# Optimization experiments

Measured on AMD Instinct MI355X. Metric: run time of the kernel, lower is better.

The kernel has to match this reference:

```python
import jax, jax.numpy as jnp
import numpy as np

NEG = -1e9

def _lstm_dir(x, w_ih, w_hh, b_ih, b_hh):
    # x: (N, T, in) -> (N, T, H); torch gate order i, f, g, o
    xi = x @ w_ih.T + (b_ih + b_hh)  # (N, T, 4H) input projection precomputed
    H = w_hh.shape[1]
    h0 = jnp.zeros((x.shape[0], H), x.dtype)
    def step(carry, xt):
        h, c = carry
        g = xt + h @ w_hh.T
        i, f, gg, o = jnp.split(g, 4, axis=-1)
        c = jax.nn.sigmoid(f) * c + jax.nn.sigmoid(i) * jnp.tanh(gg)
        h = jax.nn.sigmoid(o) * jnp.tanh(c)
        return (h, c), h
    _, ys = jax.lax.scan(step, (h0, h0), jnp.swapaxes(xi, 0, 1))
    return jnp.swapaxes(ys, 0, 1)

def _bilstm_layer(x, wif, whf, bif, bhf, wib, whb, bib, bhb):
    fwd = _lstm_dir(x, wif, whf, bif, bhf)
    bwd = _lstm_dir(x[:, ::-1], wib, whb, bib, bhb)[:, ::-1]
    return jnp.concatenate([fwd, bwd], axis=-1)

def _na1d(x, qkv_w, qkv_b, rpb, proj_w, proj_b, heads, kernel):
    # NATTEN-style 1D neighborhood attention with edge-clamped window + rel pos bias.
    N, L, Dm = x.shape
    hd = Dm // heads
    qkv = x @ qkv_w.T + qkv_b
    q, k, v = jnp.split(qkv, 3, axis=-1)
    sh = lambda t: t.reshape(N, L, heads, hd).transpose(0, 2, 1, 3)
    q, k, v = sh(q) * (hd ** -0.5), sh(k), sh(v)
    scores = jnp.einsum('nhid,nhjd->nhij', q, k)  # (N, heads, L, L)
    i = jnp.arange(L)[:, None]
    j = jnp.arange(L)[None, :]
    start = jnp.clip(i - kernel // 2, 0, L - kernel)     # window start per query
    mask = (j >= start) & (j < start + kernel)           # (L, L) neighborhood mask
    rel = jnp.clip(j - i + kernel - 1, 0, 2 * kernel - 2)
    bias = rpb[:, rel]                                   # (heads, L, L)
    scores = jnp.where(mask, scores + bias, NEG)
    attn = jax.nn.softmax(scores, axis=-1)
    out = jnp.einsum('nhij,nhjd->nhid', attn, v)
    out = out.transpose(0, 2, 1, 3).reshape(N, L, Dm)
    return out @ proj_w.T + proj_b

def setup_inputs() -> dict:
    key = jax.random.key(0)
    ks = iter(jax.random.split(key, 40))
    B, IN, T, P, Dm, H = 4, 256, 256, 88, 128, 64
    p = lambda *s: jax.random.normal(next(ks), s, jnp.float32) * 0.05
    inp = {'x': jax.random.normal(next(ks), (B, IN, T, P), jnp.float32)}
    for l, fin in (('l0', IN), ('l1', Dm)):
        for suf in ('', 'r'):
            inp['w_ih_' + l + suf] = p(4 * H, fin)
            inp['w_hh_' + l + suf] = p(4 * H, H)
            inp['b_ih_' + l + suf] = p(4 * H)
            inp['b_hh_' + l + suf] = p(4 * H)
    for tag, kz in (('t', 7), ('f', 87)):
        inp['qkv_w_' + tag] = p(3 * Dm, Dm)
        inp['qkv_b_' + tag] = p(3 * Dm)
        inp['rpb_' + tag] = p(1, 2 * kz - 1)
        inp['proj_w_' + tag] = p(Dm, Dm)
        inp['proj_b_' + tag] = p(Dm)
    return inp

def reference(x, w_ih_l0, w_hh_l0, b_ih_l0, b_hh_l0, w_ih_l0r, w_hh_l0r, b_ih_l0r, b_hh_l0r, w_ih_l1, w_hh_l1, b_ih_l1, b_hh_l1, w_ih_l1r, w_hh_l1r, b_ih_l1r, b_hh_l1r, qkv_w_t, qkv_b_t, rpb_t, proj_w_t, proj_b_t, qkv_w_f, qkv_b_f, rpb_f, proj_w_f, proj_b_f):
    B, IN, T, P = x.shape
    Dm = proj_w_t.shape[0]
    h = jnp.transpose(x, (0, 3, 2, 1)).reshape(B * P, T, IN)
    h = _bilstm_layer(h, w_ih_l0, w_hh_l0, b_ih_l0, b_hh_l0, w_ih_l0r, w_hh_l0r, b_ih_l0r, b_hh_l0r)
    h = _bilstm_layer(h, w_ih_l1, w_hh_l1, b_ih_l1, b_hh_l1, w_ih_l1r, w_hh_l1r, b_ih_l1r, b_hh_l1r)
    h = _na1d(h, qkv_w_t, qkv_b_t, rpb_t, proj_w_t, proj_b_t, 1, 7)            # time axis
    h = h.reshape(B, P, T, Dm).transpose(0, 2, 1, 3).reshape(B * T, P, Dm)
    h = _na1d(h, qkv_w_f, qkv_b_f, rpb_f, proj_w_f, proj_b_f, 1, 87)           # pitch axis
    return h.reshape(B, T, P, Dm)
```

## Files before the change

kernel.cpp:

```cpp
#include <hip/hip_runtime.h>
#include <cstdint>

#define TP 22528
#define MROWS 90112

typedef __bf16 bf16x8 __attribute__((ext_vector_type(8)));
typedef float  f32x4  __attribute__((ext_vector_type(4)));
typedef unsigned short ushort8 __attribute__((ext_vector_type(8)));

__device__ __forceinline__ unsigned short f2bf(float x) {
    unsigned u = __builtin_bit_cast(unsigned, x);
    return (unsigned short)((u + 0x7fffu + ((u >> 16) & 1u)) >> 16);
}
__device__ __forceinline__ float bf2f(unsigned short h) {
    return __builtin_bit_cast(float, (unsigned)h << 16);
}
__device__ __forceinline__ void gl16(const void* g, void* l) {
    __builtin_amdgcn_global_load_lds(
        (const __attribute__((address_space(1))) void*)g,
        (__attribute__((address_space(3))) void*)l, 16, 0, 0);
}

__global__ void convert_w(const float* __restrict__ s0, const float* __restrict__ s1,
                          const float* __restrict__ s2, const float* __restrict__ s3,
                          const float* __restrict__ s4, const float* __restrict__ s5,
                          const float* __restrict__ s6, const float* __restrict__ s7,
                          unsigned short* __restrict__ WH, unsigned short* __restrict__ WL)
{
    const int stride = gridDim.x * blockDim.x;
    for (int i = blockIdx.x * blockDim.x + threadIdx.x; i < 327680; i += stride) {
        const float* s; int base;
        if      (i <  65536) { s = s0; base = 0; }
        else if (i < 131072) { s = s1; base = 65536; }
        else if (i < 163840) { s = s2; base = 131072; }
        else if (i < 196608) { s = s3; base = 163840; }
        else if (i < 245760) { s = s4; base = 196608; }
        else if (i < 262144) { s = s5; base = 245760; }
        else if (i < 311296) { s = s6; base = 262144; }
        else                 { s = s7; base = 311296; }
        const float v = s[i - base];
        const unsigned short h = f2bf(v);
        WH[i] = h; WL[i] = f2bf(v - bf2f(h));
    }
}

__launch_bounds__(256)
__global__ void transpose_x(const float* __restrict__ x,
                            unsigned short* __restrict__ Xh,
                            unsigned short* __restrict__ Xl)
{
    __shared__ float tile[64][65];
    const int tid = threadIdx.x;
    const int tp0 = blockIdx.x * 64, k0 = blockIdx.y * 64, b = blockIdx.z;
    #pragma unroll
    for (int i = 0; i < 16; ++i) {
        const int idx = i * 256 + tid;
        const int kl = idx >> 6, tpl = idx & 63;
        tile[kl][tpl] = x[(size_t)(b * 256 + k0 + kl) * TP + tp0 + tpl];
    }
    __syncthreads();
    #pragma unroll
    for (int i = 0; i < 2; ++i) {
        const int u = i * 2048 + tid * 8;
        const int ml = u >> 6, kl0 = u & 63;
        ushort8 hi, lo;
        #pragma unroll
        for (int j = 0; j < 8; ++j) {
            const float v = tile[kl0 + j][ml];
            const unsigned short h = f2bf(v);
            hi[j] = h; lo[j] = f2bf(v - bf2f(h));
        }
        const size_t row = (size_t)b * TP + tp0 + ml;
        *(ushort8*)&Xh[row * 256 + k0 + kl0] = hi;
        *(ushort8*)&Xl[row * 256 + k0 + kl0] = lo;
    }
}

template<int OUTBF>
__launch_bounds__(256, 2)
__global__ void gemm_bf16(const unsigned short* __restrict__ Ahi,
                          const unsigned short* __restrict__ Alo,
                          const unsigned short* __restrict__ Whi0,
                          const unsigned short* __restrict__ Wlo0,
                          const unsigned short* __restrict__ Whi1,
                          const unsigned short* __restrict__ Wlo1,
                          const float* __restrict__ b0a, const float* __restrict__ b0b,
                          const float* __restrict__ b1a, const float* __restrict__ b1b,
                          float* __restrict__ C,
                          unsigned short* __restrict__ Chi, unsigned short* __restrict__ Clo,
                          int ldc, int K, int splitN, int NB)
{
    __shared__ unsigned short lds[32768];
    const int tid  = threadIdx.x;
    const int bid  = blockIdx.x;
    const int q8   = (int)gridDim.x >> 3;
    const int wq   = (bid & 7) * q8 + (bid >> 3);
    const int nb   = wq % NB;
    const int mb   = wq / NB;
    const int n0   = nb * 128;
    const int m0   = mb * 128;
    const unsigned short* Wh; const unsigned short* Wl;
    const float* ba; const float* bb; int nr0;
    if (n0 < splitN) { Wh = Whi0; Wl = Wlo0; ba = b0a; bb = b0b; nr0 = n0; }
    else             { Wh = Whi1; Wl = Wlo1; ba = b1a; bb = b1b; nr0 = n0 - splitN; }
    const int lane = tid & 63;
    const int wv   = tid >> 6;
    const int wm   = wv >> 1, wn = wv & 1;
    const int lr   = lane & 15, lg = lane >> 4;
    const int voff = (lane >> 2) * K + (((lane & 3) ^ ((lane >> 2) & 3)) * 8);
    const int wb   = wv * 1024;

    const unsigned short* gAh = Ahi + (size_t)(m0 + wv * 32) * K + voff;
    const unsigned short* gAl = Alo + (size_t)(m0 + wv * 32) * K + voff;
    const unsigned short* gBh = Wh + (size_t)(nr0 + wv * 32) * K + voff;
    const unsigned short* gBl = Wl + (size_t)(nr0 + wv * 32) * K + voff;

    const int NT = K >> 5;
    f32x4 acc[4][4] = {};

    auto stage = [&](int bufi, int ks) {
        unsigned short* base = lds + bufi * 16384;
        gl16(gAh + ks,          base +         wb);
        gl16(gAh + ks + 16 * K, base +         wb + 512);
        gl16(gAl + ks,          base + 4096  + wb);
        gl16(gAl + ks + 16 * K, base + 4096  + wb + 512);
        gl16(gBh + ks,          base + 8192  + wb);
        gl16(gBh + ks + 16 * K, base + 8192  + wb + 512);
        gl16(gBl + ks,          base + 12288 + wb);
        gl16(gBl + ks + 16 * K, base + 12288 + wb + 512);
    };

    stage(0, 0);
    for (int t = 0; t < NT; ++t) {
        const int cur = (t & 1) * 16384;
        if (t + 1 < NT) {
            stage((t & 1) ^ 1, (t + 1) * 32);
            asm volatile("s_waitcnt vmcnt(8)" ::: "memory");
        } else {
            asm volatile("s_waitcnt vmcnt(0)" ::: "memory");
        }
        __builtin_amdgcn_s_barrier();
        __builtin_amdgcn_sched_barrier(0);
        bf16x8 ah[4], al[4], bh[4], bl[4];
        #pragma unroll
        for (int mf = 0; mf < 4; ++mf) {
            const int r = wm * 64 + mf * 16 + lr;
            const int o = r * 32 + ((lg ^ (r & 3)) * 8);
            ah[mf] = *(const bf16x8*)&lds[cur + o];
            al[mf] = *(const bf16x8*)&lds[cur + 4096 + o];
        }
        #pragma unroll
        for (int nf = 0; nf < 4; ++nf) {
            const int r = wn * 64 + nf * 16 + lr;
            const int o = r * 32 + ((lg ^ (r & 3)) * 8);
            bh[nf] = *(const bf16x8*)&lds[cur + 8192 + o];
            bl[nf] = *(const bf16x8*)&lds[cur + 12288 + o];
        }
        #pragma unroll
        for (int mf = 0; mf < 4; ++mf)
            #pragma unroll
            for (int nf = 0; nf < 4; ++nf) {
                acc[mf][nf] = __builtin_amdgcn_mfma_f32_16x16x32_bf16(ah[mf], bh[nf], acc[mf][nf], 0, 0, 0);
                acc[mf][nf] = __builtin_amdgcn_mfma_f32_16x16x32_bf16(ah[mf], bl[nf], acc[mf][nf], 0, 0, 0);
                acc[mf][nf] = __builtin_amdgcn_mfma_f32_16x16x32_bf16(al[mf], bh[nf], acc[mf][nf], 0, 0, 0);
            }
        __builtin_amdgcn_s_barrier();
        __builtin_amdgcn_sched_barrier(0);
    }
    #pragma unroll
    for (int nf = 0; nf < 4; ++nf) {
        const int ncol = wn * 64 + nf * 16 + lr;
        const float bias = ba[nr0 + ncol] + (bb ? bb[nr0 + ncol] : 0.0f);
        #pragma unroll
        for (int mf = 0; mf < 4; ++mf) {
            const int row = m0 + wm * 64 + mf * 16 + lg * 4;
            #pragma unroll
            for (int i = 0; i < 4; ++i) {
                const float v = acc[mf][nf][i] + bias;
                if (OUTBF) {
                    const size_t o = (size_t)(row + i) * ldc + n0 + ncol;
                    const unsigned short h = f2bf(v);
                    Chi[o] = h; Clo[o] = f2bf(v - bf2f(h));
                } else {
                    C[(size_t)(row + i) * ldc + n0 + ncol] = v;
                }
            }
        }
    }
}

__launch_bounds__(256)
__global__ void lstm_kernel(const float* __restrict__ XI,
                            const float* __restrict__ whh_f,
                            const float* __restrict__ whh_b,
                            unsigned short* __restrict__ Hh,
                            unsigned short* __restrict__ Hl)
{
    const int bid = blockIdx.x;
    const int dir = bid & 1;
    const int n   = bid >> 1;
    const int b   = n / 88, p = n - 88 * (n / 88);
    const int j   = threadIdx.x;
    const float* whh = dir ? whh_b : whh_f;
    const int j0 = dir ? 256 : 0;
    const int ho = dir ? 64 : 0;
    float w[64];
    #pragma unroll
    for (int k = 0; k < 64; k += 4) {
        const float4 wv = *(const float4*)(whh + (size_t)j * 64 + k);
        w[k] = wv.x; w[k+1] = wv.y; w[k+2] = wv.z; w[k+3] = wv.w;
    }
    __shared__ float h_sh[64];
    __shared__ float acts[256];
    if (j < 64) h_sh[j] = 0.0f;
    float c = 0.0f;
    __syncthreads();
    const size_t rowbase = (size_t)(b * 256) * 88 + p;
    float pref = XI[(rowbase + (size_t)(dir ? 255 : 0) * 88) * 512 + j0 + j];
    for (int step = 0; step < 256; ++step) {
        const int t = dir ? (255 - step) : step;
        const size_t r = rowbase + (size_t)t * 88;
        float gs0 = pref, gs1 = 0.0f, gs2 = 0.0f, gs3 = 0.0f;
        if (step + 1 < 256) {
            const int tn = dir ? (254 - step) : (step + 1);
            pref = XI[(rowbase + (size_t)tn * 88) * 512 + j0 + j];
        }
        #pragma unroll
        for (int k = 0; k < 64; k += 16) {
            const float4 h0 = *(const float4*)&h_sh[k];
            const float4 h1 = *(const float4*)&h_sh[k + 4];
            const float4 h2 = *(const float4*)&h_sh[k + 8];
            const float4 h3 = *(const float4*)&h_sh[k + 12];
            gs0 += h0.x * w[k]    + h0.y * w[k+1]  + h0.z * w[k+2]  + h0.w * w[k+3];
            gs1 += h1.x * w[k+4]  + h1.y * w[k+5]  + h1.z * w[k+6]  + h1.w * w[k+7];
            gs2 += h2.x * w[k+8]  + h2.y * w[k+9]  + h2.z * w[k+10] + h2.w * w[k+11];
            gs3 += h3.x * w[k+12] + h3.y * w[k+13] + h3.z * w[k+14] + h3.w * w[k+15];
        }
        const float g = (gs0 + gs1) + (gs2 + gs3);
        float a;
        if (j >= 128 && j < 192) {
            const float e = __expf(2.0f * g);
            a = 1.0f - 2.0f / (e + 1.0f);
        } else {
            a = 1.0f / (1.0f + __expf(-g));
        }
        acts[j] = a;
        __syncthreads();
        if (j < 64) {
            const float ai = acts[j], af = acts[64 + j], ag = acts[128 + j], ao = acts[192 + j];
            c = af * c + ai * ag;
            const float e = __expf(2.0f * c);
            const float th = 1.0f - 2.0f / (e + 1.0f);
            const float h = ao * th;
            h_sh[j] = h;
            const size_t o = r * 128 + ho + j;
            const unsigned short hh = f2bf(h);
            Hh[o] = hh; Hl[o] = f2bf(h - bf2f(hh));
        }
        __syncthreads();
    }
}

__launch_bounds__(256)
__global__ void na_t_kernel(const float* __restrict__ QKV,
                            const float* __restrict__ rpb,
                            unsigned short* __restrict__ OUTh,
                            unsigned short* __restrict__ OUTl)
{
    const int wave = threadIdx.x >> 6;
    const int lane = threadIdx.x & 63;
    const int q = blockIdx.x * 4 + wave;
    const int b = q / TP; int rem = q - b * TP;
    const int i = rem / 88; const int p = rem - 88 * (rem / 88);
    int start = i - 3; if (start < 0) start = 0; if (start > 249) start = 249;
    const float scale = 0.08838834764831845f;
    const float* qrow = QKV + (size_t)q * 384;
    const float q0 = qrow[lane] * scale;
    const float q1 = qrow[lane + 64] * scale;
    const size_t rbase = (size_t)(b * 256) * 88 + p;
    float s[7];
    #pragma unroll
    for (int jj = 0; jj < 7; ++jj) {
        const int t = start + jj;
        const float* krow = QKV + (rbase + (size_t)t * 88) * 384 + 128;
        float part = q0 * krow[lane] + q1 * krow[lane + 64];
        part += __shfl_xor(part, 1);
        part += __shfl_xor(part, 2);
        part += __shfl_xor(part, 4);
        part += __shfl_xor(part, 8);
        part += __shfl_xor(part, 16);
        part += __shfl_xor(part, 32);
        int rel = t - i + 6; if (rel < 0) rel = 0; if (rel > 12) rel = 12;
        s[jj] = part + rpb[rel];
    }
    float m = s[0];
    #pragma unroll
    for (int jj = 1; jj < 7; ++jj) m = fmaxf(m, s[jj]);
    float sum = 0.0f;
    #pragma unroll
    for (int jj = 0; jj < 7; ++jj) { s[jj] = __expf(s[jj] - m); sum += s[jj]; }
    const float inv = 1.0f / sum;
    float o0 = 0.0f, o1 = 0.0f;
    #pragma unroll
    for (int jj = 0; jj < 7; ++jj) {
        const float* vrow = QKV + (rbase + (size_t)(start + jj) * 88) * 384 + 256;
        const float pj = s[jj] * inv;
        o0 += pj * vrow[lane];
        o1 += pj * vrow[lane + 64];
    }
    const size_t oi = (size_t)q * 128 + lane;
    const unsigned short h0 = f2bf(o0);
    OUTh[oi] = h0; OUTl[oi] = f2bf(o0 - bf2f(h0));
    const unsigned short h1 = f2bf(o1);
    OUTh[oi + 64] = h1; OUTl[oi + 64] = f2bf(o1 - bf2f(h1));
}

#define LPAD 133
#define SPAD 89
__launch_bounds__(256)
__global__ void na_f_kernel(const float* __restrict__ QKV,
                            const float* __restrict__ rpb,
                            unsigned short* __restrict__ OUTh,
                            unsigned short* __restrict__ OUTl)
{
    __shared__ float Qs[96][LPAD];
    __shared__ float Ks[96][LPAD];
    __shared__ float Ss[96][SPAD];
    const int blk = blockIdx.x;
    const int tid = threadIdx.x;
    const size_t base = (size_t)blk * 88 * 384;
    const float scale = 0.08838834764831845f;
    for (int f = tid; f < 2816; f += 256) {
        const int row = f >> 5, c4 = (f & 31) * 4;
        const float4 qv = *(const float4*)(QKV + base + (size_t)row * 384 + c4);
        Qs[row][c4+0] = qv.x * scale; Qs[row][c4+1] = qv.y * scale;
        Qs[row][c4+2] = qv.z * scale; Qs[row][c4+3] = qv.w * scale;
        const float4 kv = *(const float4*)(QKV + base + (size_t)row * 384 + 128 + c4);
        Ks[row][c4+0] = kv.x; Ks[row][c4+1] = kv.y;
        Ks[row][c4+2] = kv.z; Ks[row][c4+3] = kv.w;
    }
    __syncthreads();
    const int tx = tid & 15, ty = tid >> 4;
    {
        float acc[6][6] = {};
        for (int kk = 0; kk < 128; ++kk) {
            float a[6], bb[6];
            #pragma unroll
            for (int i = 0; i < 6; ++i) a[i] = Qs[ty*6 + i][kk];
            #pragma unroll
            for (int j = 0; j < 6; ++j) bb[j] = Ks[tx*6 + j][kk];
            #pragma unroll
            for (int i = 0; i < 6; ++i)
                #pragma unroll
                for (int j = 0; j < 6; ++j)
                    acc[i][j] += a[i] * bb[j];
        }
        #pragma unroll
        for (int i = 0; i < 6; ++i) {
            const int qq = ty*6 + i;
            if (qq < 88) {
                const int jex = (qq <= 43) ? 87 : 0;
                #pragma unroll
                for (int j = 0; j < 6; ++j) {
                    const int k = tx*6 + j;
                    if (k < 88) {
                        int rel = k - qq + 86;
                        rel = rel < 0 ? 0 : (rel > 172 ? 172 : rel);
                        Ss[qq][k] = (k == jex) ? -1e30f : acc[i][j] + rpb[rel];
                    }
                }
            }
        }
    }
    __syncthreads();
    for (int f = tid; f < 2816; f += 256) {
        const int row = f >> 5, c4 = (f & 31) * 4;
        const float4 vv = *(const float4*)(QKV + base + (size_t)row * 384 + 256 + c4);
        Ks[row][c4+0] = vv.x; Ks[row][c4+1] = vv.y;
        Ks[row][c4+2] = vv.z; Ks[row][c4+3] = vv.w;
    }
    if (tid < 176) {
        const int rrow = tid >> 1, hf = tid & 1;
        const int k0 = hf * 44;
        float m = -1e30f;
        for (int k = k0; k < k0 + 44; ++k) m = fmaxf(m, Ss[rrow][k]);
        m = fmaxf(m, __shfl_xor(m, 1));
        float sum = 0.0f;
        for (int k = k0; k < k0 + 44; ++k) {
            const float e = __expf(Ss[rrow][k] - m);
            Ss[rrow][k] = e;
            sum += e;
        }
        sum += __shfl_xor(sum, 1);
        const float inv = 1.0f / sum;
        for (int k = k0; k < k0 + 44; ++k) Ss[rrow][k] *= inv;
    }
    __syncthreads();
    {
        float o[6][8] = {};
        for (int k = 0; k < 88; ++k) {
            float pv[6], vv[8];
            #pragma unroll
            for (int i = 0; i < 6; ++i) pv[i] = Ss[ty*6 + i][k];
            #pragma unroll
            for (int j = 0; j < 8; ++j) vv[j] = Ks[k][tx + 16*j];
            #pragma unroll
            for (int i = 0; i < 6; ++i)
                #pragma unroll
                for (int j = 0; j < 8; ++j)
                    o[i][j] += pv[i] * vv[j];
        }
        #pragma unroll
        for (int i = 0; i < 6; ++i) {
            const int qq = ty*6 + i;
            if (qq < 88) {
                const size_t ro = ((size_t)blk * 88 + qq) * 128;
                #pragma unroll
                for (int j = 0; j < 8; ++j) {
                    const float v = o[i][j];
                    const unsigned short hh = f2bf(v);
                    OUTh[ro + tx + 16*j] = hh;
                    OUTl[ro + tx + 16*j] = f2bf(v - bf2f(hh));
                }
            }
        }
    }
}

extern "C" void kernel_launch(void* const* d_in, const int* in_sizes, int n_in,
                              void* d_out, int out_size, void* d_ws, size_t ws_size,
                              hipStream_t stream)
{
    const float* x         = (const float*)d_in[0];
    const float* w_ih_l0   = (const float*)d_in[1];
    const float* w_hh_l0   = (const float*)d_in[2];
    const float* b_ih_l0   = (const float*)d_in[3];
    const float* b_hh_l0   = (const float*)d_in[4];
    const float* w_ih_l0r  = (const float*)d_in[5];
    const float* w_hh_l0r  = (const float*)d_in[6];
    const float* b_ih_l0r  = (const float*)d_in[7];
    const float* b_hh_l0r  = (const float*)d_in[8];
    const float* w_ih_l1   = (const float*)d_in[9];
    const float* w_hh_l1   = (const float*)d_in[10];
    const float* b_ih_l1   = (const float*)d_in[11];
    const float* b_hh_l1   = (const float*)d_in[12];
    const float* w_ih_l1r  = (const float*)d_in[13];
    const float* w_hh_l1r  = (const float*)d_in[14];
    const float* b_ih_l1r  = (const float*)d_in[15];
    const float* b_hh_l1r  = (const float*)d_in[16];
    const float* qkv_w_t   = (const float*)d_in[17];
    const float* qkv_b_t   = (const float*)d_in[18];
    const float* rpb_t     = (const float*)d_in[19];
    const float* proj_w_t  = (const float*)d_in[20];
    const float* proj_b_t  = (const float*)d_in[21];
    const float* qkv_w_f   = (const float*)d_in[22];
    const float* qkv_b_f   = (const float*)d_in[23];
    const float* rpb_f     = (const float*)d_in[24];
    const float* proj_w_f  = (const float*)d_in[25];
    const float* proj_b_f  = (const float*)d_in[26];

    float* ws = (float*)d_ws;
    float*          XI   = ws;
    float*          QKV  = ws;
    unsigned short* ATTh = (unsigned short*)(ws + (size_t)MROWS * 384);
    unsigned short* ATTl = ATTh + (size_t)MROWS * 128;
    unsigned short* Hh   = (unsigned short*)(ws + 46137344);
    unsigned short* Hl   = Hh + (size_t)MROWS * 128;
    unsigned short* Gh   = (unsigned short*)(ws + 57671680);
    unsigned short* Gl   = Gh + (size_t)MROWS * 128;
    unsigned short* Xh   = (unsigned short*)(ws + 46137344);
    unsigned short* Xl   = Xh + (size_t)MROWS * 256;
    unsigned short* WH   = (unsigned short*)(ws + 69206016);
    unsigned short* WL   = WH + 327680;

    const int BIG = 1 << 30;
    const dim3 blk(256);

    convert_w<<<dim3(320), blk, 0, stream>>>(w_ih_l0, w_ih_l0r, w_ih_l1, w_ih_l1r,
        qkv_w_t, proj_w_t, qkv_w_f, proj_w_f, WH, WL);
    transpose_x<<<dim3(352, 4, 4), blk, 0, stream>>>(x, Xh, Xl);
    gemm_bf16<0><<<dim3(2816), blk, 0, stream>>>(Xh, Xl,
        WH, WL, WH + 65536, WL + 65536,
        b_ih_l0, b_hh_l0, b_ih_l0r, b_hh_l0r,
        XI, nullptr, nullptr, 512, 256, 256, 4);
    lstm_kernel<<<dim3(704), blk, 0, stream>>>(XI, w_hh_l0, w_hh_l0r, Hh, Hl);
    gemm_bf16<0><<<dim3(2816), blk, 0, stream>>>(Hh, Hl,
        WH + 131072, WL + 131072, WH + 163840, WL + 163840,
        b_ih_l1, b_hh_l1, b_ih_l1r, b_hh_l1r,
        XI, nullptr, nullptr, 512, 128, 256, 4);
    lstm_kernel<<<dim3(704), blk, 0, stream>>>(XI, w_hh_l1, w_hh_l1r, Hh, Hl);
    gemm_bf16<0><<<dim3(2112), blk, 0, stream>>>(Hh, Hl,
        WH + 196608, WL + 196608, WH + 196608, WL + 196608,
        qkv_b_t, nullptr, qkv_b_t, nullptr,
        QKV, nullptr, nullptr, 384, 128, BIG, 3);
    na_t_kernel<<<dim3(22528), blk, 0, stream>>>(QKV, rpb_t, ATTh, ATTl);
    gemm_bf16<1><<<dim3(704), blk, 0, stream>>>(ATTh, ATTl,
        WH + 245760, WL + 245760, WH + 245760, WL + 245760,
        proj_b_t, nullptr, proj_b_t, nullptr,
        nullptr, Gh, Gl, 128, 128, BIG, 1);
    gemm_bf16<0><<<dim3(2112), blk, 0, stream>>>(Gh, Gl,
        WH + 262144, WL + 262144, WH + 262144, WL + 262144,
        qkv_b_f, nullptr, qkv_b_f, nullptr,
        QKV, nullptr, nullptr, 384, 128, BIG, 3);
    na_f_kernel<<<dim3(1024), blk, 0, stream>>>(QKV, rpb_f, ATTh, ATTl);
    gemm_bf16<0><<<dim3(704), blk, 0, stream>>>(ATTh, ATTl,
        WH + 311296, WL + 311296, WH + 311296, WL + 311296,
        proj_b_f, nullptr, proj_b_f, nullptr,
        (float*)d_out, nullptr, nullptr, 128, 128, BIG, 1);
}
```

Baseline: 1.056 ms.

## Batch 16 LSTM sequences per block and compute recurrence with split-bf16 MFMA

Replaces the per-sequence scalar-FMA LSTM kernel with one that packs 16 sequences per block and computes the h·W_hh recurrence using bf16 MFMA, keeping fp32-like accuracy through hi/lo bf16 splitting (three products per k-chunk). The hidden state is exchanged through a double-buffered LDS tile, which needs only one barrier per step, and XI is prefetched two steps ahead. The grid shrinks from 704 to 44 blocks, so most CUs sit idle on the 256 serial steps. Per-step latency is now set by chained MFMAs plus one barrier, and the split-bf16 products carry some precision risk.

```diff
diff --git a/kernel.cpp b/kernel.cpp
--- a/kernel.cpp
+++ b/kernel.cpp
@@ -189,75 +189,124 @@
     }
 }
 
+#define UPAD 88
 __launch_bounds__(256)
-__global__ void lstm_kernel(const float* __restrict__ XI,
-                            const float* __restrict__ whh_f,
-                            const float* __restrict__ whh_b,
-                            unsigned short* __restrict__ Hh,
-                            unsigned short* __restrict__ Hl)
+__global__ void lstm_mfma(const float* __restrict__ XI,
+                          const float* __restrict__ whh_f,
+                          const float* __restrict__ whh_b,
+                          unsigned short* __restrict__ Hh,
+                          unsigned short* __restrict__ Hl)
 {
     const int bid = blockIdx.x;
     const int dir = bid & 1;
-    const int n   = bid >> 1;
-    const int b   = n / 88, p = n - 88 * (n / 88);
-    const int j   = threadIdx.x;
+    const int grp = bid >> 1;
+    const int tid = threadIdx.x;
+    const int w   = tid >> 6;
+    const int lane = tid & 63;
+    const int lr = lane & 15, lg = lane >> 4;
     const float* whh = dir ? whh_b : whh_f;
     const int j0 = dir ? 256 : 0;
     const int ho = dir ? 64 : 0;
-    float w[64];
-    #pragma unroll
-    for (int k = 0; k < 64; k += 4) {
-        const float4 wv = *(const float4*)(whh + (size_t)j * 64 + k);
-        w[k] = wv.x; w[k+1] = wv.y; w[k+2] = wv.z; w[k+3] = wv.w;
-    }
-    __shared__ float h_sh[64];
-    __shared__ float acts[256];
-    if (j < 64) h_sh[j] = 0.0f;
-    float c = 0.0f;
-    __syncthreads();
-    const size_t rowbase = (size_t)(b * 256) * 88 + p;
-    float pref = XI[(rowbase + (size_t)(dir ? 255 : 0) * 88) * 512 + j0 + j];
-    for (int step = 0; step < 256; ++step) {
+
+    int rowA[4];
+    #pragma unroll
+    for (int r = 0; r < 4; ++r) {
+        const int s = grp * 16 + lg * 4 + r;
+        const int b = s / 88;
+        rowA[r] = b * TP + (s - b * 88);
+    }
+    int rowC;
+    { const int s = grp * 16 + lr; const int b = s / 88; rowC = b * TP + (s - b * 88); }
+
+    bf16x8 wh[4][2], wl[4][2];
+    #pragma unroll
+    for (int fi = 0; fi < 4; ++fi) {
+        const int gate = fi * 64 + w * 16 + lr;
+        #pragma unroll
+        for (int ka = 0; ka < 2; ++ka) {
+            const float* src = whh + (size_t)gate * 64 + ka * 32 + lg * 8;
+            ushort8 th, tl;
+            #pragma unroll
+            for (int e = 0; e < 8; ++e) {
+                const float v = src[e];
+                const unsigned short hv = f2bf(v);
+                th[e] = hv; tl[e] = f2bf(v - bf2f(hv));
+            }
+            wh[fi][ka] = __builtin_bit_cast(bf16x8, th);
+            wl[fi][ka] = __builtin_bit_cast(bf16x8, tl);
+        }
+    }
+
+    __shared__ __attribute__((aligned(16))) unsigned short hls[2][2][16][UPAD];
+
+    bf16x8 ahh0 = {}, ahh1 = {}, ahl0 = {}, ahl1 = {};
+    f32x4 c4 = {0.0f, 0.0f, 0.0f, 0.0f};
+
+    f32x4 xiA[4], xiB[4];
+    auto xiload = [&](f32x4 (&dst)[4], int step) {
         const int t = dir ? (255 - step) : step;
-        const size_t r = rowbase + (size_t)t * 88;
-        float gs0 = pref, gs1 = 0.0f, gs2 = 0.0f, gs3 = 0.0f;
-        if (step + 1 < 256) {
-            const int tn = dir ? (254 - step) : (step + 1);
-            pref = XI[(rowbase + (size_t)tn * 88) * 512 + j0 + j];
-        }
-        #pragma unroll
-        for (int k = 0; k < 64; k += 16) {
-            const float4 h0 = *(const float4*)&h_sh[k];
-            const float4 h1 = *(const float4*)&h_sh[k + 4];
-            const float4 h2 = *(const float4*)&h_sh[k + 8];
-            const float4 h3 = *(const float4*)&h_sh[k + 12];
-            gs0 += h0.x * w[k]    + h0.y * w[k+1]  + h0.z * w[k+2]  + h0.w * w[k+3];
-            gs1 += h1.x * w[k+4]  + h1.y * w[k+5]  + h1.z * w[k+6]  + h1.w * w[k+7];
-            gs2 += h2.x * w[k+8]  + h2.y * w[k+9]  + h2.z * w[k+10] + h2.w * w[k+11];
-            gs3 += h3.x * w[k+12] + h3.y * w[k+13] + h3.z * w[k+14] + h3.w * w[k+15];
-        }
-        const float g = (gs0 + gs1) + (gs2 + gs3);
-        float a;
-        if (j >= 128 && j < 192) {
-            const float e = __expf(2.0f * g);
-            a = 1.0f - 2.0f / (e + 1.0f);
-        } else {
-            a = 1.0f / (1.0f + __expf(-g));
-        }
-        acts[j] = a;
+        #pragma unroll
+        for (int fi = 0; fi < 4; ++fi) {
+            const int col = j0 + fi * 64 + w * 16 + lr;
+            #pragma unroll
+            for (int r = 0; r < 4; ++r)
+                dst[fi][r] = XI[(size_t)(rowA[r] + t * 88) * 512 + col];
+        }
+    };
+    xiload(xiA, 0);
+    xiload(xiB, 1);
+
+    auto stepbody = [&](f32x4 (&xi)[4], int step) {
+        const int t = dir ? (255 - step) : step;
+        f32x4 acc[4];
+        #pragma unroll
+        for (int fi = 0; fi < 4; ++fi) {
+            f32x4 a = xi[fi];
+            a = __builtin_amdgcn_mfma_f32_16x16x32_bf16(ahh0, wh[fi][0], a, 0, 0, 0);
+            a = __builtin_amdgcn_mfma_f32_16x16x32_bf16(ahl0, wh[fi][0], a, 0, 0, 0);
+            a = __builtin_amdgcn_mfma_f32_16x16x32_bf16(ahh0, wl[fi][0], a, 0, 0, 0);
+            a = __builtin_amdgcn_mfma_f32_16x16x32_bf16(ahh1, wh[fi][1], a, 0, 0, 0);
+            a = __builtin_amdgcn_mfma_f32_16x16x32_bf16(ahl1, wh[fi][1], a, 0, 0, 0);
+            a = __builtin_amdgcn_mfma_f32_16x16x32_bf16(ahh1, wl[fi][1], a, 0, 0, 0);
+            acc[fi] = a;
+        }
+        if (step + 2 < 256) xiload(xi, step + 2);
+        f32x4 hv;
+        #pragma unroll
+        for (int r = 0; r < 4; ++r) {
+            const float si = 1.0f / (1.0f + __expf(-acc[0][r]));
+            const float sf = 1.0f / (1.0f + __expf(-acc[1][r]));
+            const float eg = __expf(2.0f * acc[2][r]);
+            const float tg = 1.0f - 2.0f / (eg + 1.0f);
+            const float so = 1.0f / (1.0f + __expf(-acc[3][r]));
+            c4[r] = sf * c4[r] + si * tg;
+            const float ec = __expf(2.0f * c4[r]);
+            const float tc = 1.0f - 2.0f / (ec + 1.0f);
+            hv[r] = so * tc;
+        }
+        const int bi = step & 1;
+        #pragma unroll
+        for (int r = 0; r < 4; ++r) {
+            const unsigned short hh = f2bf(hv[r]);
+            hls[bi][0][lg * 4 + r][w * 16 + lr] = hh;
+            hls[bi][1][lg * 4 + r][w * 16 + lr] = f2bf(hv[r] - bf2f(hh));
+        }
         __syncthreads();
-        if (j < 64) {
-            const float ai = acts[j], af = acts[64 + j], ag = acts[128 + j], ao = acts[192 + j];
-            c = af * c + ai * ag;
-            const float e = __expf(2.0f * c);
-            const float th = 1.0f - 2.0f / (e + 1.0f);
-            const float h = ao * th;
-            h_sh[j] = h;
-            const size_t o = r * 128 + ho + j;
-            const unsigned short hh = f2bf(h);
-            Hh[o] = hh; Hl[o] = f2bf(h - bf2f(hh));
-        }
-        __syncthreads();
+        ahh0 = *(const bf16x8*)&hls[bi][0][lr][lg * 8];
+        ahl0 = *(const bf16x8*)&hls[bi][1][lr][lg * 8];
+        ahh1 = *(const bf16x8*)&hls[bi][0][lr][32 + lg * 8];
+        ahl1 = *(const bf16x8*)&hls[bi][1][lr][32 + lg * 8];
+        if (w == 0) {
+            const size_t o = (size_t)(rowC + t * 88) * 128 + ho + lg * 8;
+            *(ushort8*)&Hh[o]      = __builtin_bit_cast(ushort8, ahh0);
+            *(ushort8*)&Hl[o]      = __builtin_bit_cast(ushort8, ahl0);
+            *(ushort8*)&Hh[o + 32] = __builtin_bit_cast(ushort8, ahh1);
+            *(ushort8*)&Hl[o + 32] = __builtin_bit_cast(ushort8, ahl1);
+        }
+    };
+    for (int st = 0; st < 256; st += 2) {
+        stepbody(xiA, st);
+        stepbody(xiB, st + 1);
     }
 }
 
@@ -483,12 +532,12 @@
         WH, WL, WH + 65536, WL + 65536,
         b_ih_l0, b_hh_l0, b_ih_l0r, b_hh_l0r,
         XI, nullptr, nullptr, 512, 256, 256, 4);
-    lstm_kernel<<<dim3(704), blk, 0, stream>>>(XI, w_hh_l0, w_hh_l0r, Hh, Hl);
+    lstm_mfma<<<dim3(44), blk, 0, stream>>>(XI, w_hh_l0, w_hh_l0r, Hh, Hl);
     gemm_bf16<0><<<dim3(2816), blk, 0, stream>>>(Hh, Hl,
         WH + 131072, WL + 131072, WH + 163840, WL + 163840,
         b_ih_l1, b_hh_l1, b_ih_l1r, b_hh_l1r,
         XI, nullptr, nullptr, 512, 128, 256, 4);
-    lstm_kernel<<<dim3(704), blk, 0, stream>>>(XI, w_hh_l1, w_hh_l1r, Hh, Hl);
+    lstm_mfma<<<dim3(44), blk, 0, stream>>>(XI, w_hh_l1, w_hh_l1r, Hh, Hl);
     gemm_bf16<0><<<dim3(2112), blk, 0, stream>>>(Hh, Hl,
         WH + 196608, WL + 196608, WH + 196608, WL + 196608,
         qkv_b_t, nullptr, qkv_b_t, nullptr,
```

New measurement: 1.294 ms. 22.5% more time.
